# Kernel optimization log

Measured on AMD Instinct MI355X. Metric: run time of the kernel, lower is better.

Reference implementation:

```python
import jax, jax.numpy as jnp
import numpy as np

EMBED_DIM = 1024
NUM_HEADS = 16
HEAD_DIM = EMBED_DIM // NUM_HEADS
B, S = 2, 2048
NEG = -1e20


def setup_inputs() -> dict:
    key = jax.random.key(0)
    ks = jax.random.split(key, 8)
    scale = 0.02
    return {
        "query": jax.random.normal(ks[0], (B, S, EMBED_DIM), jnp.float32),
        "keys": jax.random.normal(ks[1], (B, S, EMBED_DIM), jnp.float32),
        "values": jax.random.normal(ks[2], (B, S, EMBED_DIM), jnp.float32),
        "mask": jax.random.randint(ks[3], (1, 1, S, S), 0, 2, jnp.int32),
        "Wq": jax.random.normal(ks[4], (EMBED_DIM, EMBED_DIM), jnp.float32) * scale,
        "Wk": jax.random.normal(ks[5], (EMBED_DIM, EMBED_DIM), jnp.float32) * scale,
        "Wv": jax.random.normal(ks[6], (EMBED_DIM, EMBED_DIM), jnp.float32) * scale,
        "Wo": jax.random.normal(ks[7], (EMBED_DIM, EMBED_DIM), jnp.float32) * scale,
        "bo": jnp.zeros((EMBED_DIM,), jnp.float32),
    }


def reference(query, keys, values, mask, Wq, Wk, Wv, Wo, bo):
    N, Lq, _ = query.shape
    Lk = keys.shape[1]
    # torch nn.Linear: y = x @ W.T  (bias=False for Q/K/V)
    Q = (query @ Wq.T).reshape(N, Lq, NUM_HEADS, HEAD_DIM)
    K = (keys @ Wk.T).reshape(N, Lk, NUM_HEADS, HEAD_DIM)
    V = (values @ Wv.T).reshape(N, Lk, NUM_HEADS, HEAD_DIM)
    # NOTE: source scales by sqrt(embed_dim), not sqrt(head_dim) — kept faithful.
    energy = jnp.einsum("nqhd,nkhd->nhqk", Q, K) / jnp.sqrt(
        jnp.asarray(EMBED_DIM, Q.dtype)
    )
    energy = jnp.where(mask == 0, jnp.asarray(NEG, energy.dtype), energy)
    attention = jax.nn.softmax(energy, axis=3)
    out = jnp.einsum("nhqk,nkhd->nqhd", attention, V).reshape(N, Lq, EMBED_DIM)
    return out @ Wo.T + bo
```

## Files before the change

### kernel.cpp

```cpp
#include <hip/hip_runtime.h>
#include <stdint.h>

typedef __bf16 bf16;
typedef __bf16 bf16x4 __attribute__((ext_vector_type(4)));
typedef __bf16 bf16x8 __attribute__((ext_vector_type(8)));
typedef float f32x4 __attribute__((ext_vector_type(4)));
typedef float f32x16 __attribute__((ext_vector_type(16)));
typedef unsigned int uintx2 __attribute__((ext_vector_type(2)));
typedef unsigned int uintx4 __attribute__((ext_vector_type(4)));

#define MFMA16(a, b, c) __builtin_amdgcn_mfma_f32_16x16x32_bf16((a), (b), (c), 0, 0, 0)
#define MFMA32(a, b, c) __builtin_amdgcn_mfma_f32_32x32x16_bf16((a), (b), (c), 0, 0, 0)

__device__ __forceinline__ void gload16(const bf16* g, bf16* l) {
    __builtin_amdgcn_global_load_lds(
        (const __attribute__((address_space(1))) void*)g,
        (__attribute__((address_space(3))) void*)l, 16, 0, 0);
}

__device__ __forceinline__ float fast_exp2(float x) {
#if __has_builtin(__builtin_amdgcn_exp2f)
    return __builtin_amdgcn_exp2f(x);
#else
    return exp2f(x);
#endif
}

__global__ __launch_bounds__(256) void cvt_kernel(
    const float* __restrict__ q, const float* __restrict__ k, const float* __restrict__ v,
    const float* __restrict__ wq, const float* __restrict__ wk,
    const float* __restrict__ wv, const float* __restrict__ wo,
    const int* __restrict__ mask,
    bf16* __restrict__ qb, bf16* __restrict__ kb, bf16* __restrict__ vb,
    bf16* __restrict__ wqb, bf16* __restrict__ wkb, bf16* __restrict__ wvb,
    bf16* __restrict__ wob, unsigned long long* __restrict__ maskb)
{
    int z = blockIdx.z;
    if (z == 7) {
#pragma unroll
        for (int it = 0; it < 8; ++it) {
            int gid  = it * 524288 + blockIdx.x * 256 + threadIdx.x;
            int lane = gid & 63;
            int mv = mask[gid];
            unsigned long long bits = __ballot(mv != 0);
            if (lane == 0) maskb[gid >> 6] = bits;
        }
        return;
    }
    const float* src; bf16* dst; int n;
    switch (z) {
        case 0:  src = q;  dst = qb;  n = 4194304; break;
        case 1:  src = k;  dst = kb;  n = 4194304; break;
        case 2:  src = v;  dst = vb;  n = 4194304; break;
        case 3:  src = wq; dst = wqb; n = 1048576; break;
        case 4:  src = wk; dst = wkb; n = 1048576; break;
        case 5:  src = wv; dst = wvb; n = 1048576; break;
        default: src = wo; dst = wob; n = 1048576; break;
    }
    int i = (blockIdx.x * 256 + threadIdx.x) * 8;
    if (i >= n) return;
    float4 f0 = *(const float4*)(src + i);
    float4 f1 = *(const float4*)(src + i + 4);
    bf16x8 o;
    o[0] = (bf16)f0.x; o[1] = (bf16)f0.y; o[2] = (bf16)f0.z; o[3] = (bf16)f0.w;
    o[4] = (bf16)f1.x; o[5] = (bf16)f1.y; o[6] = (bf16)f1.z; o[7] = (bf16)f1.w;
    *(bf16x8*)(dst + i) = o;
}

template <int OUTMODE, int MT>
__global__ __launch_bounds__(256) void gemm_kernel(
    const bf16* __restrict__ A0, const bf16* __restrict__ A1, const bf16* __restrict__ A2,
    const bf16* __restrict__ B0, const bf16* __restrict__ B1, const bf16* __restrict__ B2,
    bf16* __restrict__ C0, bf16* __restrict__ C1, bf16* __restrict__ Vt,
    const float* __restrict__ bias, float* __restrict__ outf)
{
    constexpr int MI = (MT == 128) ? 4 : 2;
    constexpr int SMEM = (OUTMODE == 0 && MT == 128) ? (128 * 136) : (MT * 32 + 128 * 32);
    __shared__ bf16 smem[SMEM];
    bf16* At = smem;
    bf16* Bt = smem + MT * 32;

    const int z = blockIdx.z;
    const bf16* A = (z == 0) ? A0 : (z == 1) ? A1 : A2;
    const bf16* B = (z == 0) ? B0 : (z == 1) ? B1 : B2;

    const int tid  = threadIdx.x;
    const int lane = tid & 63;
    const int wave = tid >> 6;
    const int quad = lane >> 4;
    const int l16  = lane & 15;
    const int wm = (wave >> 1) * (MT / 2);
    const int wn = (wave & 1) * 64;
    const int m0 = blockIdx.y * MT;
    const int n0 = blockIdx.x * 128;

    const int lrow = lane >> 2;
    const int lcol = (lane & 3) * 8;

    f32x4 acc[MI][4] = {};

    const bf16* Ag = A + (size_t)(m0 + lrow) * 1024 + lcol;
    const bf16* Bg = B + (size_t)(n0 + lrow) * 1024 + lcol;

    for (int k0 = 0; k0 < 1024; k0 += 32) {
        __syncthreads();
        if constexpr (MT == 128) {
#pragma unroll
            for (int j = 0; j < 2; ++j)
                gload16(Ag + (size_t)(wave * 32 + j * 16) * 1024 + k0,
                        At + (wave * 32 + j * 16) * 32);
        } else {
            gload16(Ag + (size_t)(wave * 16) * 1024 + k0, At + (wave * 16) * 32);
        }
#pragma unroll
        for (int j = 0; j < 2; ++j)
            gload16(Bg + (size_t)(wave * 32 + j * 16) * 1024 + k0,
                    Bt + (wave * 32 + j * 16) * 32);
        __syncthreads();

        bf16x8 af[MI], bg[4];
#pragma unroll
        for (int i = 0; i < MI; ++i)
            af[i] = *(const bf16x8*)(At + (wm + i * 16 + l16) * 32 + quad * 8);
#pragma unroll
        for (int j = 0; j < 4; ++j)
            bg[j] = *(const bf16x8*)(Bt + (wn + j * 16 + l16) * 32 + quad * 8);
#pragma unroll
        for (int i = 0; i < MI; ++i)
#pragma unroll
            for (int j = 0; j < 4; ++j)
                acc[i][j] = MFMA16(af[i], bg[j], acc[i][j]);
    }

    if constexpr (OUTMODE == 0) {
        if (MT == 128 && z == 2) {
            __syncthreads();
            const int qsw = ((quad & 1) << 1) | (quad >> 1);
#pragma unroll
            for (int i = 0; i < MI; ++i)
#pragma unroll
                for (int j = 0; j < 4; ++j) {
                    int e  = wn + j * 16 + l16;
                    int sp = wm + i * 16 + qsw * 4;
                    bf16x4 v4;
#pragma unroll
                    for (int r = 0; r < 4; ++r) v4[r] = (bf16)acc[i][j][r];
                    *(bf16x4*)(smem + e * 136 + sp) = v4;
                }
            __syncthreads();
            const int bq = m0 >> 11;
            const int srow = m0 & 2047;
#pragma unroll
            for (int c = 0; c < 2; ++c) {
                int idx = c * 256 + tid;
                int e = idx >> 2, sc = (idx & 3) * 32;
                bf16* dst = Vt + (size_t)(bq * 1024 + n0 + e) * 2048 + srow + sc;
#pragma unroll
                for (int kk = 0; kk < 4; ++kk)
                    *(bf16x8*)(dst + kk * 8) =
                        *(const bf16x8*)(smem + e * 136 + sc + kk * 8);
            }
            return;
        }
        bf16* C = (z == 0) ? C0 : C1;
        const float cs = (z == 0) ? 0.0450842200277800f : 1.0f;
#pragma unroll
        for (int i = 0; i < MI; ++i)
#pragma unroll
            for (int j = 0; j < 4; ++j) {
                int row = m0 + wm + i * 16 + quad * 4;
                int col = n0 + wn + j * 16 + l16;
#pragma unroll
                for (int r = 0; r < 4; ++r)
                    C[(row + r) * 1024 + col] = (bf16)(acc[i][j][r] * cs);
            }
    } else {
#pragma unroll
        for (int j = 0; j < 4; ++j) {
            int col = n0 + wn + j * 16 + l16;
            float bj = bias[col];
#pragma unroll
            for (int i = 0; i < MI; ++i) {
                int row = m0 + wm + i * 16 + quad * 4;
#pragma unroll
                for (int r = 0; r < 4; ++r)
                    outf[(row + r) * 1024 + col] = acc[i][j][r] + bj;
            }
        }
    }
}

__global__ __launch_bounds__(512, 4) void flash_kernel(
    const bf16* __restrict__ Q, const bf16* __restrict__ K, const bf16* __restrict__ Vt,
    const unsigned long long* __restrict__ maskb, bf16* __restrict__ O)
{
    __shared__ char smem[65536];

    const int tid  = threadIdx.x;
    const int lane = tid & 63;
    const int wave = tid >> 6;
    const int half = wave >> 2;
    const int w4   = wave & 3;
    const int l32  = lane & 31;
    const int hl   = lane >> 5;
    const int l7   = lane & 7;

    const int flat = blockIdx.x + 16 * (blockIdx.y + 16 * blockIdx.z);
    const int xcd  = flat & 7;
    const int slot = flat >> 3;
    const int bh   = xcd * 4 + (slot >> 4);
    const int h  = bh & 15;
    const int b  = bh >> 4;
    const int q0 = (slot & 15) * 128;
    const int qt = q0 + w4 * 32;

    bf16* hbase = (bf16*)smem + half * 16384;
    bf16* K0 = hbase;
    bf16* K1 = hbase + 4096;
    bf16* V0 = hbase + 8192;
    bf16* V1 = hbase + 12288;

    const bf16* Qb = Q + (size_t)(b * 2048 + qt + l32) * 1024 + h * 64 + hl * 8;
    bf16x8 qf[4];
#pragma unroll
    for (int ks = 0; ks < 4; ++ks) qf[ks] = *(const bf16x8*)(Qb + ks * 16);

    bf16x8 ones;
#pragma unroll
    for (int j = 0; j < 8; ++j) ones[j] = (bf16)1.0f;

    f32x16 acc[2] = {};
    f32x16 lacc = {};

    const int dmarow = lane >> 3;
    const int dmacol = (l7 ^ dmarow) * 8;
    const bf16* Kg = K + (size_t)(b * 2048 + w4 * 16 + dmarow) * 1024 + h * 64 + dmacol;
    const bf16* Vg = Vt + (size_t)((b * 16 + h) * 64 + w4 * 16 + dmarow) * 2048 + dmacol;
    const unsigned long long* Mg = maskb + (size_t)(qt + l32) * 32 + half * 16;
    const int kbase = half * 1024;

    auto stage = [&](bf16* Kd, bf16* Vd, int ktAbs) {
        gload16(Kg + (size_t)ktAbs * 1024,       Kd + (w4 * 16) * 64);
        gload16(Kg + (size_t)(ktAbs + 8) * 1024, Kd + (w4 * 16 + 8) * 64);
        gload16(Vg + ktAbs,                      Vd + (w4 * 16) * 64);
        gload16(Vg + ktAbs + 8 * 2048,           Vd + (w4 * 16 + 8) * 64);
    };

    unsigned long long mw = Mg[0];
    stage(K0, V0, kbase);

    auto body = [&](const bf16* Kc, const bf16* Vc, bf16* Kn, bf16* Vn, int it) {
        __syncthreads();
        unsigned long long mw_next = 0;
        if (it + 1 < 16) {
            stage(Kn, Vn, kbase + (it + 1) * 64);
            mw_next = Mg[it + 1];
        }

        bf16x8 pa[4];
#pragma unroll
        for (int t = 0; t < 2; ++t) {
            f32x16 s = {};
            __builtin_amdgcn_s_setprio(1);
#pragma unroll
            for (int ks = 0; ks < 4; ++ks) {
                bf16x8 ka = *(const bf16x8*)(Kc + (t * 32 + l32) * 64 +
                                             (((ks * 2 + hl) ^ l7) * 8));
                s = MFMA32(ka, qf[ks], s);
            }
            __builtin_amdgcn_s_setprio(0);
            unsigned mwt = (unsigned)(mw >> (t * 32 + 4 * hl));
            unsigned W[4][2];
#pragma unroll
            for (int g = 0; g < 4; ++g) {
                bf16x4 pv;
#pragma unroll
                for (int r = 0; r < 4; ++r) {
                    float ev = fast_exp2(s[g * 4 + r]);
                    pv[r] = (mwt & (1u << (8 * g + r))) ? (bf16)ev : (bf16)0.0f;
                }
                uintx2 u = __builtin_bit_cast(uintx2, pv);
                W[g][0] = u[0];
                W[g][1] = u[1];
            }
#pragma unroll
            for (int kh = 0; kh < 2; ++kh) {
                uintx4 aw = { W[2 * kh][0], W[2 * kh][1],
                              W[2 * kh + 1][0], W[2 * kh + 1][1] };
                pa[t * 2 + kh] = __builtin_bit_cast(bf16x8, aw);
            }
        }

        __builtin_amdgcn_s_setprio(1);
#pragma unroll
        for (int dt = 0; dt < 2; ++dt)
#pragma unroll
            for (int ks = 0; ks < 4; ++ks) {
                bf16x8 vb = *(const bf16x8*)(Vc + (dt * 32 + l32) * 64 +
                                             (((ks * 2 + hl) ^ l7) * 8));
                acc[dt] = MFMA32(pa[ks], vb, acc[dt]);
            }
#pragma unroll
        for (int ks = 0; ks < 4; ++ks)
            lacc = MFMA32(pa[ks], ones, lacc);
        __builtin_amdgcn_s_setprio(0);

        mw = mw_next;
    };

    for (int it = 0; it < 16; it += 2) {
        body(K0, V0, K1, V1, it);
        body(K1, V1, K0, V0, it + 1);
    }

    __syncthreads();
    float* cb = (float*)smem;
    float* ex = cb + (w4 * 64 + lane) * 4;
    if (half == 1) {
#pragma unroll
        for (int i = 0; i < 4; ++i) {
            f32x4 t0, t1, t2;
#pragma unroll
            for (int j = 0; j < 4; ++j) {
                t0[j] = acc[0][i * 4 + j];
                t1[j] = acc[1][i * 4 + j];
                t2[j] = lacc[i * 4 + j];
            }
            *(f32x4*)(ex + (i + 0) * 1024) = t0;
            *(f32x4*)(ex + (i + 4) * 1024) = t1;
            *(f32x4*)(ex + (i + 8) * 1024) = t2;
        }
    }
    __syncthreads();
    if (half == 0) {
#pragma unroll
        for (int i = 0; i < 4; ++i) {
            f32x4 t0 = *(const f32x4*)(ex + (i + 0) * 1024);
            f32x4 t1 = *(const f32x4*)(ex + (i + 4) * 1024);
            f32x4 t2 = *(const f32x4*)(ex + (i + 8) * 1024);
#pragma unroll
            for (int j = 0; j < 4; ++j) {
                acc[0][i * 4 + j] += t0[j];
                acc[1][i * 4 + j] += t1[j];
                lacc[i * 4 + j]   += t2[j];
            }
        }

        const size_t obase = (size_t)(b * 2048 + qt) * 1024 + h * 64;
#pragma unroll
        for (int g = 0; g < 4; ++g)
#pragma unroll
            for (int r = 0; r < 4; ++r) {
                int qr = 4 * hl + 8 * g + r;
                float inv = 1.0f / lacc[g * 4 + r];
                O[obase + (size_t)qr * 1024 + l32]      = (bf16)(acc[0][g * 4 + r] * inv);
                O[obase + (size_t)qr * 1024 + 32 + l32] = (bf16)(acc[1][g * 4 + r] * inv);
            }
    }
}

extern "C" void kernel_launch(void* const* d_in, const int* in_sizes, int n_in,
                              void* d_out, int out_size, void* d_ws, size_t ws_size,
                              hipStream_t stream)
{
    const float* q  = (const float*)d_in[0];
    const float* k  = (const float*)d_in[1];
    const float* v  = (const float*)d_in[2];
    const int* mask = (const int*)d_in[3];
    const float* wq = (const float*)d_in[4];
    const float* wk = (const float*)d_in[5];
    const float* wv = (const float*)d_in[6];
    const float* wo = (const float*)d_in[7];
    const float* bo = (const float*)d_in[8];
    float* out = (float*)d_out;

    char* p = (char*)d_ws;
    auto alloc = [&](size_t bytes) {
        char* r = p;
        p += (bytes + 255) & ~(size_t)255;
        return r;
    };
    const size_t SB = (size_t)4096 * 1024 * 2;
    const size_t WB = (size_t)1024 * 1024 * 2;
    bf16* qb  = (bf16*)alloc(SB);
    bf16* kb  = (bf16*)alloc(SB);
    bf16* vb  = (bf16*)alloc(SB);
    bf16* wqb = (bf16*)alloc(WB);
    bf16* wkb = (bf16*)alloc(WB);
    bf16* wvb = (bf16*)alloc(WB);
    bf16* wob = (bf16*)alloc(WB);
    bf16* Qp  = (bf16*)alloc(SB);
    bf16* Kp  = (bf16*)alloc(SB);
    bf16* Vtp = (bf16*)alloc(SB);
    bf16* Ob  = (bf16*)alloc(SB);
    unsigned long long* maskb = (unsigned long long*)alloc(2048 * 32 * 8);

    cvt_kernel<<<dim3(2048, 1, 8), 256, 0, stream>>>(
        q, k, v, wq, wk, wv, wo, mask, qb, kb, vb, wqb, wkb, wvb, wob, maskb);

    gemm_kernel<0, 128><<<dim3(8, 32, 3), 256, 0, stream>>>(
        qb, kb, vb, wqb, wkb, wvb, Qp, Kp, Vtp, nullptr, nullptr);

    flash_kernel<<<dim3(16, 16, 2), 512, 0, stream>>>(Qp, Kp, Vtp, maskb, Ob);

    gemm_kernel<1, 64><<<dim3(8, 64, 1), 256, 0, stream>>>(
        Ob, nullptr, nullptr, wob, nullptr, nullptr,
        nullptr, nullptr, nullptr, bo, out);
}
```

Before: 233.0 us.

## Load K/V fragments directly from global in flash kernel; XCD-aware GEMM tile mapping

The flash attention kernel drops the double-buffered LDS staging of K and V tiles and has each lane read its MFMA operand fragments straight from global memory, relying on L2/L1 caching. The cross-half reduction now uses a smaller 32KB float buffer in two passes, which lowers shared memory use and may raise occupancy. The GEMM kernel remaps block indices so tiles sharing the same rows land on the same XCD for better L2 locality. The risk is that uncoalesced, unprefetched global loads in the attention inner loop add latency that was previously hidden by the async LDS pipeline.

```diff
diff --git a/kernel.cpp b/kernel.cpp
--- a/kernel.cpp
+++ b/kernel.cpp
@@ -80,7 +80,19 @@
     bf16* At = smem;
     bf16* Bt = smem + MT * 32;
 
-    const int z = blockIdx.z;
+    const int f = blockIdx.x + 8 * blockIdx.y + ((OUTMODE == 0) ? 256 * blockIdx.z : 0);
+    const int xcd = f & 7, sidx = f >> 3;
+    int z, m0, n0;
+    if constexpr (OUTMODE == 0) {
+        z  = sidx >> 5;
+        m0 = (xcd * 4 + (sidx & 3)) * MT;
+        n0 = ((sidx >> 2) & 7) * 128;
+    } else {
+        z  = 0;
+        m0 = (xcd * 8 + (sidx & 7)) * MT;
+        n0 = (sidx >> 3) * 128;
+    }
+
     const bf16* A = (z == 0) ? A0 : (z == 1) ? A1 : A2;
     const bf16* B = (z == 0) ? B0 : (z == 1) ? B1 : B2;
 
@@ -91,8 +103,6 @@
     const int l16  = lane & 15;
     const int wm = (wave >> 1) * (MT / 2);
     const int wn = (wave & 1) * 64;
-    const int m0 = blockIdx.y * MT;
-    const int n0 = blockIdx.x * 128;
 
     const int lrow = lane >> 2;
     const int lcol = (lane & 3) * 8;
@@ -194,7 +204,7 @@
     const bf16* __restrict__ Q, const bf16* __restrict__ K, const bf16* __restrict__ Vt,
     const unsigned long long* __restrict__ maskb, bf16* __restrict__ O)
 {
-    __shared__ char smem[65536];
+    __shared__ float cb[8192];
 
     const int tid  = threadIdx.x;
     const int lane = tid & 63;
@@ -203,7 +213,6 @@
     const int w4   = wave & 3;
     const int l32  = lane & 31;
     const int hl   = lane >> 5;
-    const int l7   = lane & 7;
 
     const int flat = blockIdx.x + 16 * (blockIdx.y + 16 * blockIdx.z);
     const int xcd  = flat & 7;
@@ -214,12 +223,6 @@
     const int q0 = (slot & 15) * 128;
     const int qt = q0 + w4 * 32;
 
-    bf16* hbase = (bf16*)smem + half * 16384;
-    bf16* K0 = hbase;
-    bf16* K1 = hbase + 4096;
-    bf16* V0 = hbase + 8192;
-    bf16* V1 = hbase + 12288;
-
     const bf16* Qb = Q + (size_t)(b * 2048 + qt + l32) * 1024 + h * 64 + hl * 8;
     bf16x8 qf[4];
 #pragma unroll
@@ -232,30 +235,14 @@
     f32x16 acc[2] = {};
     f32x16 lacc = {};
 
-    const int dmarow = lane >> 3;
-    const int dmacol = (l7 ^ dmarow) * 8;
-    const bf16* Kg = K + (size_t)(b * 2048 + w4 * 16 + dmarow) * 1024 + h * 64 + dmacol;
-    const bf16* Vg = Vt + (size_t)((b * 16 + h) * 64 + w4 * 16 + dmarow) * 2048 + dmacol;
+    const bf16* Kh = K + ((size_t)(b * 2048 + l32)) * 1024 + h * 64 + hl * 8;
+    const bf16* Vh = Vt + ((size_t)(b * 16 + h) * 64 + l32) * 2048 + hl * 8;
     const unsigned long long* Mg = maskb + (size_t)(qt + l32) * 32 + half * 16;
     const int kbase = half * 1024;
 
-    auto stage = [&](bf16* Kd, bf16* Vd, int ktAbs) {
-        gload16(Kg + (size_t)ktAbs * 1024,       Kd + (w4 * 16) * 64);
-        gload16(Kg + (size_t)(ktAbs + 8) * 1024, Kd + (w4 * 16 + 8) * 64);
-        gload16(Vg + ktAbs,                      Vd + (w4 * 16) * 64);
-        gload16(Vg + ktAbs + 8 * 2048,           Vd + (w4 * 16 + 8) * 64);
-    };
-
-    unsigned long long mw = Mg[0];
-    stage(K0, V0, kbase);
-
-    auto body = [&](const bf16* Kc, const bf16* Vc, bf16* Kn, bf16* Vn, int it) {
-        __syncthreads();
-        unsigned long long mw_next = 0;
-        if (it + 1 < 16) {
-            stage(Kn, Vn, kbase + (it + 1) * 64);
-            mw_next = Mg[it + 1];
-        }
+    for (int it = 0; it < 16; ++it) {
+        const int kt = kbase + it * 64;
+        const unsigned long long mw = Mg[it];
 
         bf16x8 pa[4];
 #pragma unroll
@@ -264,8 +251,7 @@
             __builtin_amdgcn_s_setprio(1);
 #pragma unroll
             for (int ks = 0; ks < 4; ++ks) {
-                bf16x8 ka = *(const bf16x8*)(Kc + (t * 32 + l32) * 64 +
-                                             (((ks * 2 + hl) ^ l7) * 8));
+                bf16x8 ka = *(const bf16x8*)(Kh + (size_t)(kt + t * 32) * 1024 + ks * 16);
                 s = MFMA32(ka, qf[ks], s);
             }
             __builtin_amdgcn_s_setprio(0);
@@ -296,39 +282,28 @@
         for (int dt = 0; dt < 2; ++dt)
 #pragma unroll
             for (int ks = 0; ks < 4; ++ks) {
-                bf16x8 vb = *(const bf16x8*)(Vc + (dt * 32 + l32) * 64 +
-                                             (((ks * 2 + hl) ^ l7) * 8));
+                bf16x8 vb = *(const bf16x8*)(Vh + (size_t)(dt * 32) * 2048 + kt + ks * 16);
                 acc[dt] = MFMA32(pa[ks], vb, acc[dt]);
             }
 #pragma unroll
         for (int ks = 0; ks < 4; ++ks)
             lacc = MFMA32(pa[ks], ones, lacc);
         __builtin_amdgcn_s_setprio(0);
-
-        mw = mw_next;
-    };
-
-    for (int it = 0; it < 16; it += 2) {
-        body(K0, V0, K1, V1, it);
-        body(K1, V1, K0, V0, it + 1);
-    }
-
+    }
+
+    float* ex = cb + (w4 * 64 + lane) * 4;
     __syncthreads();
-    float* cb = (float*)smem;
-    float* ex = cb + (w4 * 64 + lane) * 4;
     if (half == 1) {
 #pragma unroll
         for (int i = 0; i < 4; ++i) {
-            f32x4 t0, t1, t2;
+            f32x4 t0, t2;
 #pragma unroll
             for (int j = 0; j < 4; ++j) {
                 t0[j] = acc[0][i * 4 + j];
-                t1[j] = acc[1][i * 4 + j];
                 t2[j] = lacc[i * 4 + j];
             }
             *(f32x4*)(ex + (i + 0) * 1024) = t0;
-            *(f32x4*)(ex + (i + 4) * 1024) = t1;
-            *(f32x4*)(ex + (i + 8) * 1024) = t2;
+            *(f32x4*)(ex + (i + 4) * 1024) = t2;
         }
     }
     __syncthreads();
@@ -336,14 +311,31 @@
 #pragma unroll
         for (int i = 0; i < 4; ++i) {
             f32x4 t0 = *(const f32x4*)(ex + (i + 0) * 1024);
-            f32x4 t1 = *(const f32x4*)(ex + (i + 4) * 1024);
-            f32x4 t2 = *(const f32x4*)(ex + (i + 8) * 1024);
+            f32x4 t2 = *(const f32x4*)(ex + (i + 4) * 1024);
 #pragma unroll
             for (int j = 0; j < 4; ++j) {
                 acc[0][i * 4 + j] += t0[j];
-                acc[1][i * 4 + j] += t1[j];
                 lacc[i * 4 + j]   += t2[j];
             }
+        }
+    }
+    __syncthreads();
+    if (half == 1) {
+#pragma unroll
+        for (int i = 0; i < 4; ++i) {
+            f32x4 t1;
+#pragma unroll
+            for (int j = 0; j < 4; ++j) t1[j] = acc[1][i * 4 + j];
+            *(f32x4*)(ex + i * 1024) = t1;
+        }
+    }
+    __syncthreads();
+    if (half == 0) {
+#pragma unroll
+        for (int i = 0; i < 4; ++i) {
+            f32x4 t1 = *(const f32x4*)(ex + i * 1024);
+#pragma unroll
+            for (int j = 0; j < 4; ++j) acc[1][i * 4 + j] += t1[j];
         }
 
         const size_t obase = (size_t)(b * 2048 + qt) * 1024 + h * 64;
```

After: 307.3 us. 1.32x slower.

## Double-buffer GEMM LDS loads, remap blocks per XCD, and use branchless mask select

Applied to the files above, without the earlier changes.

The GEMM kernel now double-buffers its A/B tiles in shared memory, so the next k-slice is issued before the current one is computed. This removes one barrier per iteration and overlaps global loads with MFMA work. Block indices are remapped so that consecutive M tiles stay on the same XCD for L2 locality, and the output projection moves from 64-row to 128-row tiles, halving its grid. The flash kernel replaces the per-element conditional select of masked probabilities with a sign-extended bitmask AND. The risk is that the output GEMM now launches fewer blocks and each uses more registers, which may reduce occupancy.

```diff
diff --git a/kernel.cpp b/kernel.cpp
--- a/kernel.cpp
+++ b/kernel.cpp
@@ -67,20 +67,26 @@
     *(bf16x8*)(dst + i) = o;
 }
 
-template <int OUTMODE, int MT>
+template <int OUTMODE>
 __global__ __launch_bounds__(256) void gemm_kernel(
     const bf16* __restrict__ A0, const bf16* __restrict__ A1, const bf16* __restrict__ A2,
     const bf16* __restrict__ B0, const bf16* __restrict__ B1, const bf16* __restrict__ B2,
     bf16* __restrict__ C0, bf16* __restrict__ C1, bf16* __restrict__ Vt,
     const float* __restrict__ bias, float* __restrict__ outf)
 {
-    constexpr int MI = (MT == 128) ? 4 : 2;
-    constexpr int SMEM = (OUTMODE == 0 && MT == 128) ? (128 * 136) : (MT * 32 + 128 * 32);
+    constexpr int SMEM = (OUTMODE == 0) ? (128 * 136) : 16384;
     __shared__ bf16 smem[SMEM];
-    bf16* At = smem;
-    bf16* Bt = smem + MT * 32;
-
-    const int z = blockIdx.z;
+    bf16* At0 = smem;
+    bf16* At1 = smem + 4096;
+    bf16* Bt0 = smem + 8192;
+    bf16* Bt1 = smem + 12288;
+
+    const int f = blockIdx.x + 8 * blockIdx.y + ((OUTMODE == 0) ? 256 * blockIdx.z : 0);
+    const int xcd = f & 7, sidx = f >> 3;
+    const int z  = sidx >> 5;
+    const int m0 = (xcd * 4 + (sidx & 3)) * 128;
+    const int n0 = ((sidx >> 2) & 7) * 128;
+
     const bf16* A = (z == 0) ? A0 : (z == 1) ? A1 : A2;
     const bf16* B = (z == 0) ? B0 : (z == 1) ? B1 : B2;
 
@@ -89,55 +95,58 @@
     const int wave = tid >> 6;
     const int quad = lane >> 4;
     const int l16  = lane & 15;
-    const int wm = (wave >> 1) * (MT / 2);
+    const int wm = (wave >> 1) * 64;
     const int wn = (wave & 1) * 64;
-    const int m0 = blockIdx.y * MT;
-    const int n0 = blockIdx.x * 128;
 
     const int lrow = lane >> 2;
     const int lcol = (lane & 3) * 8;
 
-    f32x4 acc[MI][4] = {};
+    f32x4 acc[4][4] = {};
 
     const bf16* Ag = A + (size_t)(m0 + lrow) * 1024 + lcol;
     const bf16* Bg = B + (size_t)(n0 + lrow) * 1024 + lcol;
 
-    for (int k0 = 0; k0 < 1024; k0 += 32) {
-        __syncthreads();
-        if constexpr (MT == 128) {
-#pragma unroll
-            for (int j = 0; j < 2; ++j)
-                gload16(Ag + (size_t)(wave * 32 + j * 16) * 1024 + k0,
-                        At + (wave * 32 + j * 16) * 32);
-        } else {
-            gload16(Ag + (size_t)(wave * 16) * 1024 + k0, At + (wave * 16) * 32);
-        }
+    auto stage = [&](bf16* Atb, bf16* Btb, int k0) {
+#pragma unroll
+        for (int j = 0; j < 2; ++j)
+            gload16(Ag + (size_t)(wave * 32 + j * 16) * 1024 + k0,
+                    Atb + (wave * 32 + j * 16) * 32);
 #pragma unroll
         for (int j = 0; j < 2; ++j)
             gload16(Bg + (size_t)(wave * 32 + j * 16) * 1024 + k0,
-                    Bt + (wave * 32 + j * 16) * 32);
+                    Btb + (wave * 32 + j * 16) * 32);
+    };
+
+    auto body = [&](const bf16* Ac, const bf16* Bc, bf16* An, bf16* Bn, int k0) {
         __syncthreads();
-
-        bf16x8 af[MI], bg[4];
-#pragma unroll
-        for (int i = 0; i < MI; ++i)
-            af[i] = *(const bf16x8*)(At + (wm + i * 16 + l16) * 32 + quad * 8);
+        if (k0 + 32 < 1024) stage(An, Bn, k0 + 32);
+
+        bf16x8 af[4], bg[4];
+#pragma unroll
+        for (int i = 0; i < 4; ++i)
+            af[i] = *(const bf16x8*)(Ac + (wm + i * 16 + l16) * 32 + quad * 8);
 #pragma unroll
         for (int j = 0; j < 4; ++j)
-            bg[j] = *(const bf16x8*)(Bt + (wn + j * 16 + l16) * 32 + quad * 8);
-#pragma unroll
-        for (int i = 0; i < MI; ++i)
+            bg[j] = *(const bf16x8*)(Bc + (wn + j * 16 + l16) * 32 + quad * 8);
+#pragma unroll
+        for (int i = 0; i < 4; ++i)
 #pragma unroll
             for (int j = 0; j < 4; ++j)
                 acc[i][j] = MFMA16(af[i], bg[j], acc[i][j]);
+    };
+
+    stage(At0, Bt0, 0);
+    for (int k0 = 0; k0 < 1024; k0 += 64) {
+        body(At0, Bt0, At1, Bt1, k0);
+        body(At1, Bt1, At0, Bt0, k0 + 32);
     }
 
     if constexpr (OUTMODE == 0) {
-        if (MT == 128 && z == 2) {
+        if (z == 2) {
             __syncthreads();
             const int qsw = ((quad & 1) << 1) | (quad >> 1);
 #pragma unroll
-            for (int i = 0; i < MI; ++i)
+            for (int i = 0; i < 4; ++i)
 #pragma unroll
                 for (int j = 0; j < 4; ++j) {
                     int e  = wn + j * 16 + l16;
@@ -165,7 +174,7 @@
         bf16* C = (z == 0) ? C0 : C1;
         const float cs = (z == 0) ? 0.0450842200277800f : 1.0f;
 #pragma unroll
-        for (int i = 0; i < MI; ++i)
+        for (int i = 0; i < 4; ++i)
 #pragma unroll
             for (int j = 0; j < 4; ++j) {
                 int row = m0 + wm + i * 16 + quad * 4;
@@ -180,7 +189,7 @@
             int col = n0 + wn + j * 16 + l16;
             float bj = bias[col];
 #pragma unroll
-            for (int i = 0; i < MI; ++i) {
+            for (int i = 0; i < 4; ++i) {
                 int row = m0 + wm + i * 16 + quad * 4;
 #pragma unroll
                 for (int r = 0; r < 4; ++r)
@@ -277,7 +286,9 @@
 #pragma unroll
                 for (int r = 0; r < 4; ++r) {
                     float ev = fast_exp2(s[g * 4 + r]);
-                    pv[r] = (mwt & (1u << (8 * g + r))) ? (bf16)ev : (bf16)0.0f;
+                    unsigned msk = (unsigned)((int)(mwt << (31 - (8 * g + r))) >> 31);
+                    unsigned evu = __builtin_bit_cast(unsigned, ev) & msk;
+                    pv[r] = (bf16)__builtin_bit_cast(float, evu);
                 }
                 uintx2 u = __builtin_bit_cast(uintx2, pv);
                 W[g][0] = u[0];
@@ -398,12 +409,12 @@
     cvt_kernel<<<dim3(2048, 1, 8), 256, 0, stream>>>(
         q, k, v, wq, wk, wv, wo, mask, qb, kb, vb, wqb, wkb, wvb, wob, maskb);
 
-    gemm_kernel<0, 128><<<dim3(8, 32, 3), 256, 0, stream>>>(
+    gemm_kernel<0><<<dim3(8, 32, 3), 256, 0, stream>>>(
         qb, kb, vb, wqb, wkb, wvb, Qp, Kp, Vtp, nullptr, nullptr);
 
     flash_kernel<<<dim3(16, 16, 2), 512, 0, stream>>>(Qp, Kp, Vtp, maskb, Ob);
 
-    gemm_kernel<1, 64><<<dim3(8, 64, 1), 256, 0, stream>>>(
+    gemm_kernel<1><<<dim3(8, 32, 1), 256, 0, stream>>>(
         Ob, nullptr, nullptr, wob, nullptr, nullptr,
         nullptr, nullptr, nullptr, bo, out);
 }
```

Measured after the change: 233.7 us. No clear change (+0.3%).
